# Kernel tuning notes

Measured on AMD Instinct MI355X. Metric: run time of the kernel, lower is better.

Reference implementation:

```python
import jax, jax.numpy as jnp
import numpy as np

EMB = 512
HEADS = 8
HEAD_DIM = EMB // HEADS
GN_EPS = 1e-6
THETA_SCALE = 10000.0


def _multiply_by_i(x):
    # interleave: out[..., 2i] = -x[..., 2i+1], out[..., 2i+1] = x[..., 2i]
    return jnp.stack((-x[..., 1::2], x[..., ::2]), axis=-1).reshape(x.shape)


def _theta_shift(x, sin, cos):
    return x * cos + _multiply_by_i(x) * sin


def setup_inputs() -> dict:
    key = jax.random.key(0)
    ks = jax.random.split(key, 13)
    B, N, E = 2, 2048, EMB

    def xavier(k, out_dim, in_dim):
        std = (2.0 / (out_dim + in_dim)) ** 0.5
        return std * jax.random.normal(k, (out_dim, in_dim), dtype=jnp.float32)

    return {
        "query": jax.random.normal(ks[0], (B, N, E), dtype=jnp.float32),
        "k": jax.random.normal(ks[1], (B, N, E), dtype=jnp.float32),
        "v": jax.random.normal(ks[2], (B, N, E), dtype=jnp.float32),
        "Wq": xavier(ks[3], E, E), "bq": jnp.zeros((E,), jnp.float32),
        "Wk": xavier(ks[4], E, E), "bk": jnp.zeros((E,), jnp.float32),
        "Wv": xavier(ks[5], E, E), "bv": jnp.zeros((E,), jnp.float32),
        "Wg": xavier(ks[6], E, E), "bg": jnp.zeros((E,), jnp.float32),
        "Wo": xavier(ks[7], E, E), "bo": jnp.zeros((E,), jnp.float32),
    }


def reference(query, k, v, Wq, bq, Wk, bk, Wv, bv, Wg, bg, Wo, bo):
    B, N, E = query.shape
    H, D = HEADS, E // HEADS

    def proj(x, W, b):  # torch Linear: x @ W.T + b, then split heads -> [b h n d]
        return (x @ W.T + b).reshape(B, N, H, D).transpose(0, 2, 1, 3)

    q = proj(query, Wq, bq)
    kk = proj(k, Wk, bk)
    vv = proj(v, Wv, bv)

    # rotary-style theta shift; thetas repeated pairwise [t0,t0,t1,t1,...]
    thetas = jnp.repeat(1.0 / THETA_SCALE ** jnp.linspace(0.0, 1.0, D // 2), 2)
    angles = jnp.arange(N, dtype=jnp.float32)[:, None] * thetas[None, :]  # [n d]
    sin = jnp.sin(angles)[None, None]
    cos = jnp.cos(angles)[None, None]
    q = _theta_shift(q, sin, cos)
    kk = _theta_shift(kk, sin, cos)

    # decay-masked retention (softmax-free)
    gammas = 1.0 - jnp.exp(jnp.linspace(np.log(1 / 32), np.log(1 / 512), H)).astype(jnp.float32)
    pos = jnp.arange(N)
    dist = jnp.abs(pos[:, None] - pos[None, :]).astype(jnp.float32)
    causal = pos[:, None] >= pos[None, :]
    decay_mask = jnp.where(causal[None], gammas[:, None, None] ** dist[None], 0.0)  # [h n s]

    kk = kk / (D ** 0.5)
    sim = jnp.einsum('bhnd,bhsd->bhns', q, kk) * decay_mask[None]  # [b h n n]
    ret = jnp.einsum('bhns,bhsd->bhnd', sim, vv)

    # GroupNorm(groups=H, channels=H, affine=False) over (b n) samples -> per-(b,h,n) norm over d
    mean = ret.mean(axis=-1, keepdims=True)
    var = ret.var(axis=-1, keepdims=True)
    ret = (ret - mean) / jnp.sqrt(var + GN_EPS)

    ret = ret.transpose(0, 2, 1, 3).reshape(B, N, E)
    gate = jax.nn.silu(query @ Wg.T + bg)
    out = (ret * gate) @ Wo.T + bo
    return out
```

## Files before the change

### kernel.cpp

```cpp
#include <hip/hip_runtime.h>
#include <math.h>

typedef float f32x4 __attribute__((ext_vector_type(4)));
typedef short s16x8 __attribute__((ext_vector_type(8)));
typedef short s16x4 __attribute__((ext_vector_type(4)));

__device__ __forceinline__ short f2bf(float f) {
    unsigned u = __builtin_bit_cast(unsigned, f);
    unsigned r = u + 0x7FFFu + ((u >> 16) & 1u);
    return (short)(r >> 16);
}
__device__ __forceinline__ float bf2f(short h) {
    return __builtin_bit_cast(float, ((unsigned)(unsigned short)h) << 16);
}
__device__ __forceinline__ unsigned pack2(short a, short b) {
    return (unsigned)(unsigned short)a | ((unsigned)(unsigned short)b << 16);
}

__device__ __forceinline__ void split16v(const float* __restrict__ p,
                                         short* __restrict__ h,
                                         short* __restrict__ l) {
    f32x4 a0 = *(const f32x4*)(p);
    f32x4 a1 = *(const f32x4*)(p + 4);
    f32x4 a2 = *(const f32x4*)(p + 8);
    f32x4 a3 = *(const f32x4*)(p + 12);
    #pragma unroll
    for (int i = 0; i < 4; ++i) {
        short t0;
        t0 = f2bf(a0[i]); h[i]      = t0; l[i]      = f2bf(a0[i] - bf2f(t0));
        t0 = f2bf(a1[i]); h[4 + i]  = t0; l[4 + i]  = f2bf(a1[i] - bf2f(t0));
        t0 = f2bf(a2[i]); h[8 + i]  = t0; l[8 + i]  = f2bf(a2[i] - bf2f(t0));
        t0 = f2bf(a3[i]); h[12 + i] = t0; l[12 + i] = f2bf(a3[i] - bf2f(t0));
    }
}

__device__ __forceinline__ void gload16(const void* g, void* l) {
    __builtin_amdgcn_global_load_lds(
        (const __attribute__((address_space(1))) unsigned int*)g,
        (__attribute__((address_space(3))) unsigned int*)l,
        16, 0, 0);
}

__global__ __launch_bounds__(256) void presplit_kernel(
    const float* __restrict__ W0, const float* __restrict__ W1,
    const float* __restrict__ W2, const float* __restrict__ W3,
    const float* __restrict__ W4,
    const float* __restrict__ X0, const float* __restrict__ X1,
    const float* __restrict__ X2,
    short* __restrict__ Wsp, short* __restrict__ Xsp)
{
    const int blk = blockIdx.x;
    const int t = threadIdx.x;
    short hbuf[16], lbuf[16];
    if (blk < 256) {
        const int w = blk >> 6, bi = blk & 63;
        const float* src = (w == 0) ? W0 : (w == 1) ? W1 : (w == 2) ? W2 : W3;
        const int idx = (bi * 256 + t) * 16;
        const int row = idx >> 9, k0 = idx & 511;
        const int ntile = row >> 7, r = row & 127;
        const int kstep = k0 >> 5, kk0 = k0 & 31;
        const int s = (r & 3) << 4;
        split16v(src + idx, hbuf, lbuf);
        short* hp = Wsp + (long)w * 524288 + (ntile * 16 + kstep) * 8192 + r * 32;
        short* lp = hp + 4096;
        const int oA = ((2 * kk0) ^ s) >> 1;
        const int oB = ((2 * kk0 + 16) ^ s) >> 1;
        *(s16x8*)(hp + oA) = *(s16x8*)(hbuf);
        *(s16x8*)(hp + oB) = *(s16x8*)(hbuf + 8);
        *(s16x8*)(lp + oA) = *(s16x8*)(lbuf);
        *(s16x8*)(lp + oB) = *(s16x8*)(lbuf + 8);
    } else if (blk < 320) {
        const int bi = blk - 256;
        const int idx = (bi * 256 + t) * 16;
        short* hi = Wsp + (long)4 * 524288;
        short* lo = hi + 262144;
        split16v(W4 + idx, hbuf, lbuf);
        *(s16x8*)(hi + idx)     = *(s16x8*)(hbuf);
        *(s16x8*)(hi + idx + 8) = *(s16x8*)(hbuf + 8);
        *(s16x8*)(lo + idx)     = *(s16x8*)(lbuf);
        *(s16x8*)(lo + idx + 8) = *(s16x8*)(lbuf + 8);
    } else {
        const int b2 = blk - 320;
        const int x = b2 >> 9, bi = b2 & 511;
        const float* src = (x == 0) ? X0 : (x == 1) ? X1 : X2;
        const int idx = (bi * 256 + t) * 16;
        const int row = idx >> 9, k0 = idx & 511;
        const int mtile = row >> 6, r = row & 63;
        const int kstep = k0 >> 5, kk0 = k0 & 31;
        const int s = (r & 3) << 4;
        split16v(src + idx, hbuf, lbuf);
        short* hp = Xsp + (long)x * 4194304 + (mtile * 16 + kstep) * 4096 + r * 32;
        short* lp = hp + 2048;
        const int oA = ((2 * kk0) ^ s) >> 1;
        const int oB = ((2 * kk0 + 16) ^ s) >> 1;
        *(s16x8*)(hp + oA) = *(s16x8*)(hbuf);
        *(s16x8*)(hp + oB) = *(s16x8*)(hbuf + 8);
        *(s16x8*)(lp + oA) = *(s16x8*)(lbuf);
        *(s16x8*)(lp + oB) = *(s16x8*)(lbuf + 8);
    }
}

__global__ __launch_bounds__(256, 2) void projqkvg_kernel(
    const short* __restrict__ Xsp, const short* __restrict__ Wsp,
    const float* __restrict__ bq, const float* __restrict__ bk,
    const float* __restrict__ bv, const float* __restrict__ bg,
    short* __restrict__ Qh, short* __restrict__ Ql,
    short* __restrict__ Kh, short* __restrict__ Vth,
    float* __restrict__ G)
{
    __shared__ __align__(16) short SB[36864];

    const int fid = blockIdx.x + 4 * (blockIdx.y + 64 * blockIdx.z);
    const int mtile = fid & 63;
    const int rr = fid >> 6;
    const int mode = rr & 3;
    const int ntile = rr >> 2;
    const int m0 = mtile * 64, n0 = ntile * 128;

    const int xi = (mode == 1) ? 1 : (mode == 2) ? 2 : 0;
    const float* bias = (mode == 0) ? bq : (mode == 1) ? bk
                       : (mode == 2) ? bv : bg;

    const int t = threadIdx.x, lane = t & 63, wv = t >> 6;
    const int wm = wv >> 1, wn = wv & 1;
    const int quad = lane >> 4, l15 = lane & 15;

    const short* Xblk = Xsp + (long)xi * 4194304 + (long)mtile * 16 * 4096;
    const short* Wblk = Wsp + (long)mode * 524288 + (long)ntile * 16 * 8192;

    const int c0 = wv * 6;
    const short* gs[6];
    int gstp[6];
    #pragma unroll
    for (int i = 0; i < 6; ++i) {
        const int c = c0 + i;
        const bool isx = (c < 8);
        gs[i]   = isx ? (Xblk + c * 512 + lane * 8)
                      : (Wblk + (c - 8) * 512 + lane * 8);
        gstp[i] = isx ? 4096 : 8192;
    }

    auto STAGE = [&](int stg, int ks) {
        char* dstb = (char*)SB + stg * 24576 + c0 * 1024;
        #pragma unroll
        for (int i = 0; i < 6; ++i)
            gload16(gs[i] + ks * gstp[i], dstb + i * 1024);
    };

    const int sxw = (l15 & 3) << 4;
    int aoff[2], boff[4];
    #pragma unroll
    for (int s2 = 0; s2 < 2; ++s2)
        aoff[s2] = (wm * 32 + s2 * 16 + l15) * 64 + ((quad * 16) ^ sxw);
    #pragma unroll
    for (int s2 = 0; s2 < 4; ++s2)
        boff[s2] = 8192 + (wn * 64 + s2 * 16 + l15) * 64 + ((quad * 16) ^ sxw);

    f32x4 acc[2][4];
    #pragma unroll
    for (int i = 0; i < 2; ++i)
        #pragma unroll
        for (int j = 0; j < 4; ++j)
            acc[i][j] = (f32x4){0.f, 0.f, 0.f, 0.f};

    STAGE(0, 0);
    STAGE(1, 1);
    asm volatile("s_waitcnt vmcnt(6)" ::: "memory");
    __builtin_amdgcn_s_barrier();

    int cur = 0;
    for (int ks = 0; ks < 16; ++ks) {
        if (ks < 14) {
            int fill = cur + 2; if (fill >= 3) fill -= 3;
            STAGE(fill, ks + 2);
        }
        __builtin_amdgcn_sched_barrier(0);

        const char* stg = (const char*)SB + cur * 24576;
        s16x8 ah[2], al[2], bh[4], bl[4];
        #pragma unroll
        for (int s2 = 0; s2 < 2; ++s2) {
            ah[s2] = *(const s16x8*)(stg + aoff[s2]);
            al[s2] = *(const s16x8*)(stg + 4096 + aoff[s2]);
        }
        #pragma unroll
        for (int s2 = 0; s2 < 4; ++s2) {
            bh[s2] = *(const s16x8*)(stg + boff[s2]);
            bl[s2] = *(const s16x8*)(stg + 8192 + boff[s2]);
        }
        #pragma unroll
        for (int i = 0; i < 2; ++i)
            #pragma unroll
            for (int j = 0; j < 4; ++j) {
                acc[i][j] = __builtin_amdgcn_mfma_f32_16x16x32_bf16(ah[i], bh[j], acc[i][j], 0, 0, 0);
                acc[i][j] = __builtin_amdgcn_mfma_f32_16x16x32_bf16(al[i], bh[j], acc[i][j], 0, 0, 0);
                acc[i][j] = __builtin_amdgcn_mfma_f32_16x16x32_bf16(ah[i], bl[j], acc[i][j], 0, 0, 0);
            }

        if (ks < 14)       asm volatile("s_waitcnt vmcnt(6)" ::: "memory");
        else if (ks == 14) asm volatile("s_waitcnt vmcnt(0)" ::: "memory");
        __builtin_amdgcn_sched_barrier(0);
        __builtin_amdgcn_s_barrier();

        cur += 1; if (cur >= 3) cur -= 3;
    }

    __syncthreads();

    const int bb = m0 >> 11, posb = m0 & 2047;

    if (mode == 0) {
        short* Thi = SB + wv * 2304;
        short* Tlo = Thi + 1152;
        const int hcol = (n0 >> 6) + wn;
        #pragma unroll
        for (int ms = 0; ms < 2; ++ms) {
            #pragma unroll
            for (int ns = 0; ns < 4; ++ns) {
                const int col = n0 + wn * 64 + ns * 16 + l15;
                const float bvv = bias[col];
                const int pp = (col & 63) >> 1;
                const float theta = powf(10000.0f, -(float)pp * (1.0f / 31.0f));
                #pragma unroll
                for (int r = 0; r < 4; ++r) {
                    const int m = m0 + wm * 32 + ms * 16 + quad * 4 + r;
                    const int pos = m & 2047;
                    float x = acc[ms][ns][r] + bvv;
                    float prt = __shfl_xor(x, 1);
                    float ang = (float)pos * theta;
                    float sv = sinf(ang), cv = cosf(ang);
                    float y0 = x * cv - prt * sv;
                    float y1 = prt * cv + x * sv;
                    if (!(l15 & 1)) {
                        short h0 = f2bf(y0), h1 = f2bf(y1);
                        short l0 = f2bf(y0 - bf2f(h0)), l1 = f2bf(y1 - bf2f(h1));
                        const int o = (quad * 4 + r) * 72 + ns * 16 + l15;
                        *(unsigned*)&Thi[o] = pack2(h0, h1);
                        *(unsigned*)&Tlo[o] = pack2(l0, l1);
                    }
                }
            }
            const int mrow = wm * 32 + ms * 16;
            #pragma unroll
            for (int p2 = 0; p2 < 2; ++p2) {
                const int row = p2 * 8 + (lane >> 3);
                const int ch = (lane & 7) * 8;
                s16x8 vh = *(const s16x8*)&Thi[row * 72 + ch];
                s16x8 vl = *(const s16x8*)&Tlo[row * 72 + ch];
                const long o = ((long)(bb * 8 + hcol) * 2048 + posb + mrow + row) * 64 + ch;
                *(s16x8*)(Qh + o) = vh;
                *(s16x8*)(Ql + o) = vl;
            }
        }
    } else if (mode == 1) {
        short* Thi = SB + wv * 1152;
        const int hcol = (n0 >> 6) + wn;
        #pragma unroll
        for (int ms = 0; ms < 2; ++ms) {
            #pragma unroll
            for (int ns = 0; ns < 4; ++ns) {
                const int col = n0 + wn * 64 + ns * 16 + l15;
                const float bvv = bias[col];
                const int pp = (col & 63) >> 1;
                const float theta = powf(10000.0f, -(float)pp * (1.0f / 31.0f));
                #pragma unroll
                for (int r = 0; r < 4; ++r) {
                    const int m = m0 + wm * 32 + ms * 16 + quad * 4 + r;
                    const int pos = m & 2047;
                    float x = acc[ms][ns][r] + bvv;
                    float prt = __shfl_xor(x, 1);
                    float ang = (float)pos * theta;
                    float sv = sinf(ang), cv = cosf(ang);
                    float y0 = (x * cv - prt * sv) * 0.125f;
                    float y1 = (prt * cv + x * sv) * 0.125f;
                    if (!(l15 & 1)) {
                        const int o = (quad * 4 + r) * 72 + ns * 16 + l15;
                        *(unsigned*)&Thi[o] = pack2(f2bf(y0), f2bf(y1));
                    }
                }
            }
            const int mrow = wm * 32 + ms * 16;
            #pragma unroll
            for (int p2 = 0; p2 < 2; ++p2) {
                const int row = p2 * 8 + (lane >> 3);
                const int ch = (lane & 7) * 8;
                s16x8 vh = *(const s16x8*)&Thi[row * 72 + ch];
                const long o = ((long)(bb * 8 + hcol) * 2048 + posb + mrow + row) * 64 + ch;
                *(s16x8*)(Kh + o) = vh;
            }
        }
    } else if (mode == 2) {
        short* T2 = SB;
        #pragma unroll
        for (int ns = 0; ns < 4; ++ns) {
            const int col = n0 + wn * 64 + ns * 16 + l15;
            const float bvv = bias[col];
            #pragma unroll
            for (int ms = 0; ms < 2; ++ms) {
                s16x4 pk;
                #pragma unroll
                for (int r = 0; r < 4; ++r)
                    pk[r] = f2bf(acc[ms][ns][r] + bvv);
                *(s16x4*)&T2[(wn * 64 + ns * 16 + l15) * 72
                             + wm * 32 + ms * 16 + quad * 4] = pk;
            }
        }
        __syncthreads();
        #pragma unroll
        for (int pass = 0; pass < 4; ++pass) {
            const int row = pass * 32 + (t >> 3);
            const int ch = (t & 7) * 8;
            s16x8 v = *(const s16x8*)&T2[row * 72 + ch];
            const int head = (n0 >> 6) + (row >> 6);
            const int d = row & 63;
            const long o = ((long)(bb * 8 + head) * 64 + d) * 2048 + posb + ch;
            *(s16x8*)(Vth + o) = v;
        }
    } else {
        #pragma unroll
        for (int ns = 0; ns < 4; ++ns) {
            const int col = n0 + wn * 64 + ns * 16 + l15;
            const float bvv = bias[col];
            #pragma unroll
            for (int ms = 0; ms < 2; ++ms)
                #pragma unroll
                for (int r = 0; r < 4; ++r) {
                    const int m = m0 + wm * 32 + ms * 16 + quad * 4 + r;
                    float x = acc[ms][ns][r] + bvv;
                    G[(long)m * 512 + col] = x / (1.0f + expf(-x));
                }
        }
    }
}

__global__ __launch_bounds__(256) void attn_kernel(
    const short* __restrict__ Qh_g, const short* __restrict__ Ql_g,
    const short* __restrict__ Kh_g, const short* __restrict__ Vth_g,
    const float* __restrict__ G,
    short* __restrict__ RGh)
{
    __shared__ __align__(16) short KhS[64 * 72], VhS[64 * 72];
    __shared__ __align__(16) short PhS[64 * 68];

    const int t = threadIdx.x, lane = t & 63, wv = t >> 6;
    const int quad = lane >> 4, l15 = lane & 15;
    const int bh = blockIdx.y, h = bh & 7, b = bh >> 3;
    const int qt = (bh & 1) ? blockIdx.x : (31 - blockIdx.x);
    const int n0 = qt * 64;
    const long base = (long)bh * 2048 * 64;

    float l2g;
    int stLo;
    {
        float lg0 = logf(1.0f / 32.0f), lg1 = logf(1.0f / 512.0f);
        float om = expf(lg0 + (float)h * (lg1 - lg0) * (1.0f / 7.0f));
        l2g = log2f(1.0f - om);
        int Dcut = (int)(11.5129255f / om) + 64;
        stLo = (n0 - Dcut) >> 6;
        if (stLo < 0) stLo = 0;
    }
    float gneg[16];
    #pragma unroll
    for (int i = 0; i < 16; ++i)
        gneg[i] = exp2f(-(float)((i >> 2) * 16 + (i & 3)) * l2g);

    const int srow = t >> 2;
    const int scol = (t & 3) * 16;
    const int n = n0 + wv * 16 + l15;

    s16x8 qh[2], ql[2];
    {
        const short* qp  = Qh_g + base + (long)(n0 + wv * 16 + l15) * 64 + quad * 8;
        const short* qp2 = Ql_g + base + (long)(n0 + wv * 16 + l15) * 64 + quad * 8;
        qh[0] = *(const s16x8*)qp;
        qh[1] = *(const s16x8*)(qp + 32);
        ql[0] = *(const s16x8*)qp2;
        ql[1] = *(const s16x8*)(qp2 + 32);
    }

    f32x4 racc[4];
    #pragma unroll
    for (int i = 0; i < 4; ++i) racc[i] = (f32x4){0.f, 0.f, 0.f, 0.f};

    s16x8 pk0, pk1, pv0, pv1;
    {
        const long ko = base + (long)(stLo * 64 + srow) * 64 + scol;
        pk0 = *(const s16x8*)(Kh_g + ko);
        pk1 = *(const s16x8*)(Kh_g + ko + 8);
        const long vo = base + (long)srow * 2048 + stLo * 64 + scol;
        pv0 = *(const s16x8*)(Vth_g + vo);
        pv1 = *(const s16x8*)(Vth_g + vo + 8);
    }

    for (int st = stLo; st <= qt; ++st) {
        const int s0 = st * 64;
        __syncthreads();
        *(s16x8*)&KhS[srow * 72 + scol]     = pk0;
        *(s16x8*)&KhS[srow * 72 + scol + 8] = pk1;
        *(s16x8*)&VhS[srow * 72 + scol]     = pv0;
        *(s16x8*)&VhS[srow * 72 + scol + 8] = pv1;
        __syncthreads();

        if (st < qt) {
            const long ko = base + (long)(s0 + 64 + srow) * 64 + scol;
            pk0 = *(const s16x8*)(Kh_g + ko);
            pk1 = *(const s16x8*)(Kh_g + ko + 8);
            const long vo = base + (long)srow * 2048 + s0 + 64 + scol;
            pv0 = *(const s16x8*)(Vth_g + vo);
            pv1 = *(const s16x8*)(Vth_g + vo + 8);
        }

        const float t0 = exp2f((float)(n - s0 - quad * 4) * l2g);

        #pragma unroll
        for (int sub = 0; sub < 4; ++sub) {
            const int ro = (sub * 16 + l15) * 72 + quad * 8;
            s16x8 kh0 = *(const s16x8*)&KhS[ro];
            s16x8 kh1 = *(const s16x8*)&KhS[ro + 32];
            f32x4 sacc = (f32x4){0.f, 0.f, 0.f, 0.f};
            sacc = __builtin_amdgcn_mfma_f32_16x16x32_bf16(kh0, qh[0], sacc, 0, 0, 0);
            sacc = __builtin_amdgcn_mfma_f32_16x16x32_bf16(kh1, qh[1], sacc, 0, 0, 0);
            sacc = __builtin_amdgcn_mfma_f32_16x16x32_bf16(kh0, ql[0], sacc, 0, 0, 0);
            sacc = __builtin_amdgcn_mfma_f32_16x16x32_bf16(kh1, ql[1], sacc, 0, 0, 0);

            const int sb = s0 + sub * 16 + quad * 4;
            s16x4 pkh;
            #pragma unroll
            for (int r = 0; r < 4; ++r) {
                const int s = sb + r;
                const float wgt = (n >= s) ? t0 * gneg[sub * 4 + r] : 0.0f;
                pkh[r] = f2bf(sacc[r] * wgt);
            }
            *(s16x4*)&PhS[(wv * 16 + l15) * 68 + sub * 16 + quad * 4] = pkh;
        }

        const int pro = (wv * 16 + l15) * 68 + quad * 8;
        s16x8 ph0 = *(const s16x8*)&PhS[pro];
        s16x8 ph1 = *(const s16x8*)&PhS[pro + 32];
        #pragma unroll
        for (int ds = 0; ds < 4; ++ds) {
            const int ro = (ds * 16 + l15) * 72 + quad * 8;
            s16x8 vh0 = *(const s16x8*)&VhS[ro];
            s16x8 vh1 = *(const s16x8*)&VhS[ro + 32];
            racc[ds] = __builtin_amdgcn_mfma_f32_16x16x32_bf16(ph0, vh0, racc[ds], 0, 0, 0);
            racc[ds] = __builtin_amdgcn_mfma_f32_16x16x32_bf16(ph1, vh1, racc[ds], 0, 0, 0);
        }
    }

    float mean[4], rstd[4];
    #pragma unroll
    for (int r = 0; r < 4; ++r) {
        float s = racc[0][r] + racc[1][r] + racc[2][r] + racc[3][r];
        s += __shfl_xor(s, 1); s += __shfl_xor(s, 2);
        s += __shfl_xor(s, 4); s += __shfl_xor(s, 8);
        mean[r] = s * (1.0f / 64.0f);
        float vs = 0.f;
        #pragma unroll
        for (int ds = 0; ds < 4; ++ds) {
            float d = racc[ds][r] - mean[r];
            vs += d * d;
        }
        vs += __shfl_xor(vs, 1); vs += __shfl_xor(vs, 2);
        vs += __shfl_xor(vs, 4); vs += __shfl_xor(vs, 8);
        rstd[r] = rsqrtf(vs * (1.0f / 64.0f) + 1e-6f);
    }

    __syncthreads();
    short* rgH = KhS + wv * 1152;
    #pragma unroll
    for (int ds = 0; ds < 4; ++ds) {
        #pragma unroll
        for (int r = 0; r < 4; ++r) {
            const int nn = n0 + wv * 16 + quad * 4 + r;
            const int d = ds * 16 + l15;
            const long gi = ((long)(b * 2048 + nn)) * 512 + h * 64 + d;
            float rg = (racc[ds][r] - mean[r]) * rstd[r] * G[gi];
            float prt = __shfl_xor(rg, 1);
            if (!(l15 & 1)) {
                const int o = (quad * 4 + r) * 72 + ds * 16 + l15;
                *(unsigned*)&rgH[o] = pack2(f2bf(rg), f2bf(prt));
            }
        }
    }
    #pragma unroll
    for (int p2 = 0; p2 < 2; ++p2) {
        const int row = p2 * 8 + (lane >> 3);
        const int ch = (lane & 7) * 8;
        s16x8 vh = *(const s16x8*)&rgH[row * 72 + ch];
        const int nn = n0 + wv * 16 + row;
        const long o = ((long)(b * 2048 + nn)) * 512 + h * 64 + ch;
        *(s16x8*)(RGh + o) = vh;
    }
}

__global__ __launch_bounds__(256) void projo_kernel(
    const short* __restrict__ RGh, const short* __restrict__ Woh_g,
    const float* __restrict__ bo, float* __restrict__ out)
{
    __shared__ __align__(16) char PB[23040];
    short* XhS = (short*)PB;
    short* WhS = XhS + 1280;
    short* WlS = XhS + 6400;

    const short* Wol_g = Woh_g + 262144;
    const int t = threadIdx.x, lane = t & 63, wv = t >> 6;
    const int wm = wv >> 1, wn = wv & 1;
    const int quad = lane >> 4, l15 = lane & 15;
    const int m0 = blockIdx.y * 32, n0 = blockIdx.x * 128;

    f32x4 acc[4];
    #pragma unroll
    for (int j = 0; j < 4; ++j) acc[j] = (f32x4){0.f, 0.f, 0.f, 0.f};

    const int xrow = t >> 3, xcol = (t & 7) * 4;
    const int wrow = t >> 1, wcol = (t & 1) * 16;
    const long xbase = (long)(m0 + xrow) * 512 + xcol;
    const long wbase = (long)(n0 + wrow) * 512 + wcol;

    s16x4 px;
    s16x8 pw0, pw1, pw2, pw3;
    px  = *(const s16x4*)(RGh + xbase);
    pw0 = *(const s16x8*)(Woh_g + wbase);
    pw1 = *(const s16x8*)(Woh_g + wbase + 8);
    pw2 = *(const s16x8*)(Wol_g + wbase);
    pw3 = *(const s16x8*)(Wol_g + wbase + 8);

    for (int k0 = 0; k0 < 512; k0 += 32) {
        __syncthreads();
        *(s16x4*)&XhS[xrow * 40 + xcol]     = px;
        *(s16x8*)&WhS[wrow * 40 + wcol]     = pw0;
        *(s16x8*)&WhS[wrow * 40 + wcol + 8] = pw1;
        *(s16x8*)&WlS[wrow * 40 + wcol]     = pw2;
        *(s16x8*)&WlS[wrow * 40 + wcol + 8] = pw3;
        __syncthreads();

        if (k0 + 32 < 512) {
            const long xo = xbase + k0 + 32;
            const long wo = wbase + k0 + 32;
            px  = *(const s16x4*)(RGh + xo);
            pw0 = *(const s16x8*)(Woh_g + wo);
            pw1 = *(const s16x8*)(Woh_g + wo + 8);
            pw2 = *(const s16x8*)(Wol_g + wo);
            pw3 = *(const s16x8*)(Wol_g + wo + 8);
        }

        s16x8 ah, bh[4], bl[4];
        {
            const int ro = (wm * 16 + l15) * 40 + quad * 8;
            ah = *(const s16x8*)&XhS[ro];
        }
        #pragma unroll
        for (int s = 0; s < 4; ++s) {
            const int ro = (wn * 64 + s * 16 + l15) * 40 + quad * 8;
            bh[s] = *(const s16x8*)&WhS[ro];
            bl[s] = *(const s16x8*)&WlS[ro];
        }
        #pragma unroll
        for (int j = 0; j < 4; ++j) {
            acc[j] = __builtin_amdgcn_mfma_f32_16x16x32_bf16(ah, bh[j], acc[j], 0, 0, 0);
            acc[j] = __builtin_amdgcn_mfma_f32_16x16x32_bf16(ah, bl[j], acc[j], 0, 0, 0);
        }
    }

    __syncthreads();
    float* T = (float*)PB + wv * 1152;
    #pragma unroll
    for (int ns = 0; ns < 4; ++ns) {
        const int col = n0 + wn * 64 + ns * 16 + l15;
        const float bvv = bo[col];
        #pragma unroll
        for (int r = 0; r < 4; ++r)
            T[(quad * 4 + r) * 72 + ns * 16 + l15] = acc[ns][r] + bvv;
    }
    #pragma unroll
    for (int it = 0; it < 2; ++it) {
        const int row = it * 8 + (lane >> 3);
        const int ch = (lane & 7) * 8;
        f32x4 a = *(const f32x4*)&T[row * 72 + ch];
        f32x4 c = *(const f32x4*)&T[row * 72 + ch + 4];
        const long o = (long)(m0 + wm * 16 + row) * 512 + n0 + wn * 64 + ch;
        *(f32x4*)(out + o) = a;
        *(f32x4*)(out + o + 4) = c;
    }
}

extern "C" void kernel_launch(void* const* d_in, const int* in_sizes, int n_in,
                              void* d_out, int out_size, void* d_ws, size_t ws_size,
                              hipStream_t stream) {
    const float* query = (const float*)d_in[0];
    const float* kin   = (const float*)d_in[1];
    const float* vin   = (const float*)d_in[2];
    const float* Wq = (const float*)d_in[3];
    const float* bq = (const float*)d_in[4];
    const float* Wk = (const float*)d_in[5];
    const float* bk = (const float*)d_in[6];
    const float* Wv = (const float*)d_in[7];
    const float* bv = (const float*)d_in[8];
    const float* Wg = (const float*)d_in[9];
    const float* bg = (const float*)d_in[10];
    const float* Wo = (const float*)d_in[11];
    const float* bo = (const float*)d_in[12];

    short* S = (short*)d_ws;
    const long NE = 2097152;
    short* WSp = S;
    short* Xsp = S + 2621440;
    short* Qh  = Xsp + 12582912;
    short* Ql  = Qh + NE;
    short* Kh  = Ql + NE;
    short* Vth = Kh + NE;
    float* G   = (float*)(Vth + NE);
    short* RGh = (short*)(G + NE);

    presplit_kernel<<<1856, 256, 0, stream>>>(
        Wq, Wk, Wv, Wg, Wo, query, kin, vin, WSp, Xsp);
    projqkvg_kernel<<<dim3(4, 64, 4), 256, 0, stream>>>(
        Xsp, WSp, bq, bk, bv, bg, Qh, Ql, Kh, Vth, G);
    attn_kernel<<<dim3(32, 16), 256, 0, stream>>>(
        Qh, Ql, Kh, Vth, G, RGh);
    projo_kernel<<<dim3(4, 128), 256, 0, stream>>>(
        RGh, WSp + 4 * 524288, bo, (float*)d_out);
}
```

Measured before the change: 221.0 us.

## Double projection block to 8 waves and precompute rotary sin/cos table

The QKVG projection kernel now runs 512 threads (8 waves) per block, each wave computing a 32x32 sub-tile and staging 3 instead of 6 global-to-LDS loads. MFMA sections are wrapped in s_setprio to favour matrix issue, and the per-element powf/sinf/cosf in the rotary epilogue is replaced by a lookup into a cos/sin table built by extra presplit blocks. The aim is more latency hiding and a cheaper epilogue, at the cost of an extra table read per element and a deeper per-block barrier.

```diff
diff --git a/kernel.cpp b/kernel.cpp
--- a/kernel.cpp
+++ b/kernel.cpp
@@ -47,7 +47,8 @@
     const float* __restrict__ W4,
     const float* __restrict__ X0, const float* __restrict__ X1,
     const float* __restrict__ X2,
-    short* __restrict__ Wsp, short* __restrict__ Xsp)
+    short* __restrict__ Wsp, short* __restrict__ Xsp,
+    float2* __restrict__ SC)
 {
     const int blk = blockIdx.x;
     const int t = threadIdx.x;
@@ -79,7 +80,7 @@
         *(s16x8*)(hi + idx + 8) = *(s16x8*)(hbuf + 8);
         *(s16x8*)(lo + idx)     = *(s16x8*)(lbuf);
         *(s16x8*)(lo + idx + 8) = *(s16x8*)(lbuf + 8);
-    } else {
+    } else if (blk < 1856) {
         const int b2 = blk - 320;
         const int x = b2 >> 9, bi = b2 & 511;
         const float* src = (x == 0) ? X0 : (x == 1) ? X1 : X2;
@@ -97,13 +98,20 @@
         *(s16x8*)(hp + oB) = *(s16x8*)(hbuf + 8);
         *(s16x8*)(lp + oA) = *(s16x8*)(lbuf);
         *(s16x8*)(lp + oB) = *(s16x8*)(lbuf + 8);
-    }
-}
-
-__global__ __launch_bounds__(256, 2) void projqkvg_kernel(
+    } else {
+        const int gid = (blk - 1856) * 256 + t;
+        const int pos = gid >> 5, pp = gid & 31;
+        const float theta = powf(10000.0f, -(float)pp * (1.0f / 31.0f));
+        const float ang = (float)pos * theta;
+        SC[gid] = make_float2(cosf(ang), sinf(ang));
+    }
+}
+
+__global__ __launch_bounds__(512, 4) void projqkvg_kernel(
     const short* __restrict__ Xsp, const short* __restrict__ Wsp,
     const float* __restrict__ bq, const float* __restrict__ bk,
     const float* __restrict__ bv, const float* __restrict__ bg,
+    const float2* __restrict__ SC,
     short* __restrict__ Qh, short* __restrict__ Ql,
     short* __restrict__ Kh, short* __restrict__ Vth,
     float* __restrict__ G)
@@ -122,17 +130,17 @@
                        : (mode == 2) ? bv : bg;
 
     const int t = threadIdx.x, lane = t & 63, wv = t >> 6;
-    const int wm = wv >> 1, wn = wv & 1;
+    const int wm = wv >> 2, wn = wv & 3;
     const int quad = lane >> 4, l15 = lane & 15;
 
     const short* Xblk = Xsp + (long)xi * 4194304 + (long)mtile * 16 * 4096;
     const short* Wblk = Wsp + (long)mode * 524288 + (long)ntile * 16 * 8192;
 
-    const int c0 = wv * 6;
-    const short* gs[6];
-    int gstp[6];
-    #pragma unroll
-    for (int i = 0; i < 6; ++i) {
+    const int c0 = wv * 3;
+    const short* gs[3];
+    int gstp[3];
+    #pragma unroll
+    for (int i = 0; i < 3; ++i) {
         const int c = c0 + i;
         const bool isx = (c < 8);
         gs[i]   = isx ? (Xblk + c * 512 + lane * 8)
@@ -143,29 +151,29 @@
     auto STAGE = [&](int stg, int ks) {
         char* dstb = (char*)SB + stg * 24576 + c0 * 1024;
         #pragma unroll
-        for (int i = 0; i < 6; ++i)
+        for (int i = 0; i < 3; ++i)
             gload16(gs[i] + ks * gstp[i], dstb + i * 1024);
     };
 
     const int sxw = (l15 & 3) << 4;
-    int aoff[2], boff[4];
+    int aoff[2], boff[2];
     #pragma unroll
     for (int s2 = 0; s2 < 2; ++s2)
         aoff[s2] = (wm * 32 + s2 * 16 + l15) * 64 + ((quad * 16) ^ sxw);
     #pragma unroll
-    for (int s2 = 0; s2 < 4; ++s2)
-        boff[s2] = 8192 + (wn * 64 + s2 * 16 + l15) * 64 + ((quad * 16) ^ sxw);
-
-    f32x4 acc[2][4];
+    for (int s2 = 0; s2 < 2; ++s2)
+        boff[s2] = 8192 + (wn * 32 + s2 * 16 + l15) * 64 + ((quad * 16) ^ sxw);
+
+    f32x4 acc[2][2];
     #pragma unroll
     for (int i = 0; i < 2; ++i)
         #pragma unroll
-        for (int j = 0; j < 4; ++j)
+        for (int j = 0; j < 2; ++j)
             acc[i][j] = (f32x4){0.f, 0.f, 0.f, 0.f};
 
     STAGE(0, 0);
     STAGE(1, 1);
-    asm volatile("s_waitcnt vmcnt(6)" ::: "memory");
+    asm volatile("s_waitcnt vmcnt(3)" ::: "memory");
     __builtin_amdgcn_s_barrier();
 
     int cur = 0;
@@ -177,27 +185,29 @@
         __builtin_amdgcn_sched_barrier(0);
 
         const char* stg = (const char*)SB + cur * 24576;
-        s16x8 ah[2], al[2], bh[4], bl[4];
+        s16x8 ah[2], al[2], bh[2], bl[2];
         #pragma unroll
         for (int s2 = 0; s2 < 2; ++s2) {
             ah[s2] = *(const s16x8*)(stg + aoff[s2]);
             al[s2] = *(const s16x8*)(stg + 4096 + aoff[s2]);
         }
         #pragma unroll
-        for (int s2 = 0; s2 < 4; ++s2) {
+        for (int s2 = 0; s2 < 2; ++s2) {
             bh[s2] = *(const s16x8*)(stg + boff[s2]);
             bl[s2] = *(const s16x8*)(stg + 8192 + boff[s2]);
         }
+        __builtin_amdgcn_s_setprio(1);
         #pragma unroll
         for (int i = 0; i < 2; ++i)
             #pragma unroll
-            for (int j = 0; j < 4; ++j) {
+            for (int j = 0; j < 2; ++j) {
                 acc[i][j] = __builtin_amdgcn_mfma_f32_16x16x32_bf16(ah[i], bh[j], acc[i][j], 0, 0, 0);
                 acc[i][j] = __builtin_amdgcn_mfma_f32_16x16x32_bf16(al[i], bh[j], acc[i][j], 0, 0, 0);
                 acc[i][j] = __builtin_amdgcn_mfma_f32_16x16x32_bf16(ah[i], bl[j], acc[i][j], 0, 0, 0);
             }
-
-        if (ks < 14)       asm volatile("s_waitcnt vmcnt(6)" ::: "memory");
+        __builtin_amdgcn_s_setprio(0);
+
+        if (ks < 14)       asm volatile("s_waitcnt vmcnt(3)" ::: "memory");
         else if (ks == 14) asm volatile("s_waitcnt vmcnt(0)" ::: "memory");
         __builtin_amdgcn_sched_barrier(0);
         __builtin_amdgcn_s_barrier();
@@ -210,90 +220,80 @@
     const int bb = m0 >> 11, posb = m0 & 2047;
 
     if (mode == 0) {
-        short* Thi = SB + wv * 2304;
-        short* Tlo = Thi + 1152;
-        const int hcol = (n0 >> 6) + wn;
+        short* Thi = SB + wv * 1280;
+        short* Tlo = Thi + 640;
+        const int head = (n0 >> 6) + (wn >> 1);
+        const int dbase = (wn & 1) * 32;
         #pragma unroll
         for (int ms = 0; ms < 2; ++ms) {
             #pragma unroll
-            for (int ns = 0; ns < 4; ++ns) {
-                const int col = n0 + wn * 64 + ns * 16 + l15;
+            for (int ns = 0; ns < 2; ++ns) {
+                const int col = n0 + wn * 32 + ns * 16 + l15;
                 const float bvv = bias[col];
                 const int pp = (col & 63) >> 1;
-                const float theta = powf(10000.0f, -(float)pp * (1.0f / 31.0f));
                 #pragma unroll
                 for (int r = 0; r < 4; ++r) {
                     const int m = m0 + wm * 32 + ms * 16 + quad * 4 + r;
                     const int pos = m & 2047;
                     float x = acc[ms][ns][r] + bvv;
                     float prt = __shfl_xor(x, 1);
-                    float ang = (float)pos * theta;
-                    float sv = sinf(ang), cv = cosf(ang);
-                    float y0 = x * cv - prt * sv;
-                    float y1 = prt * cv + x * sv;
+                    float2 sc = SC[pos * 32 + pp];
+                    float y0 = x * sc.x - prt * sc.y;
+                    float y1 = prt * sc.x + x * sc.y;
                     if (!(l15 & 1)) {
                         short h0 = f2bf(y0), h1 = f2bf(y1);
                         short l0 = f2bf(y0 - bf2f(h0)), l1 = f2bf(y1 - bf2f(h1));
-                        const int o = (quad * 4 + r) * 72 + ns * 16 + l15;
+                        const int o = (quad * 4 + r) * 40 + ns * 16 + l15;
                         *(unsigned*)&Thi[o] = pack2(h0, h1);
                         *(unsigned*)&Tlo[o] = pack2(l0, l1);
                     }
                 }
             }
             const int mrow = wm * 32 + ms * 16;
-            #pragma unroll
-            for (int p2 = 0; p2 < 2; ++p2) {
-                const int row = p2 * 8 + (lane >> 3);
-                const int ch = (lane & 7) * 8;
-                s16x8 vh = *(const s16x8*)&Thi[row * 72 + ch];
-                s16x8 vl = *(const s16x8*)&Tlo[row * 72 + ch];
-                const long o = ((long)(bb * 8 + hcol) * 2048 + posb + mrow + row) * 64 + ch;
-                *(s16x8*)(Qh + o) = vh;
-                *(s16x8*)(Ql + o) = vl;
-            }
+            const int row = lane >> 2, ch = (lane & 3) * 8;
+            s16x8 vh = *(const s16x8*)&Thi[row * 40 + ch];
+            s16x8 vl = *(const s16x8*)&Tlo[row * 40 + ch];
+            const long o = ((long)(bb * 8 + head) * 2048 + posb + mrow + row) * 64 + dbase + ch;
+            *(s16x8*)(Qh + o) = vh;
+            *(s16x8*)(Ql + o) = vl;
         }
     } else if (mode == 1) {
-        short* Thi = SB + wv * 1152;
-        const int hcol = (n0 >> 6) + wn;
+        short* Thi = SB + wv * 640;
+        const int head = (n0 >> 6) + (wn >> 1);
+        const int dbase = (wn & 1) * 32;
         #pragma unroll
         for (int ms = 0; ms < 2; ++ms) {
             #pragma unroll
-            for (int ns = 0; ns < 4; ++ns) {
-                const int col = n0 + wn * 64 + ns * 16 + l15;
+            for (int ns = 0; ns < 2; ++ns) {
+                const int col = n0 + wn * 32 + ns * 16 + l15;
                 const float bvv = bias[col];
                 const int pp = (col & 63) >> 1;
-                const float theta = powf(10000.0f, -(float)pp * (1.0f / 31.0f));
                 #pragma unroll
                 for (int r = 0; r < 4; ++r) {
                     const int m = m0 + wm * 32 + ms * 16 + quad * 4 + r;
                     const int pos = m & 2047;
                     float x = acc[ms][ns][r] + bvv;
                     float prt = __shfl_xor(x, 1);
-                    float ang = (float)pos * theta;
-                    float sv = sinf(ang), cv = cosf(ang);
-                    float y0 = (x * cv - prt * sv) * 0.125f;
-                    float y1 = (prt * cv + x * sv) * 0.125f;
+                    float2 sc = SC[pos * 32 + pp];
+                    float y0 = (x * sc.x - prt * sc.y) * 0.125f;
+                    float y1 = (prt * sc.x + x * sc.y) * 0.125f;
                     if (!(l15 & 1)) {
-                        const int o = (quad * 4 + r) * 72 + ns * 16 + l15;
+                        const int o = (quad * 4 + r) * 40 + ns * 16 + l15;
                         *(unsigned*)&Thi[o] = pack2(f2bf(y0), f2bf(y1));
                     }
                 }
             }
             const int mrow = wm * 32 + ms * 16;
-            #pragma unroll
-            for (int p2 = 0; p2 < 2; ++p2) {
-                const int row = p2 * 8 + (lane >> 3);
-                const int ch = (lane & 7) * 8;
-                s16x8 vh = *(const s16x8*)&Thi[row * 72 + ch];
-                const long o = ((long)(bb * 8 + hcol) * 2048 + posb + mrow + row) * 64 + ch;
-                *(s16x8*)(Kh + o) = vh;
-            }
+            const int row = lane >> 2, ch = (lane & 3) * 8;
+            s16x8 vh = *(const s16x8*)&Thi[row * 40 + ch];
+            const long o = ((long)(bb * 8 + head) * 2048 + posb + mrow + row) * 64 + dbase + ch;
+            *(s16x8*)(Kh + o) = vh;
         }
     } else if (mode == 2) {
         short* T2 = SB;
         #pragma unroll
-        for (int ns = 0; ns < 4; ++ns) {
-            const int col = n0 + wn * 64 + ns * 16 + l15;
+        for (int ns = 0; ns < 2; ++ns) {
+            const int col = n0 + wn * 32 + ns * 16 + l15;
             const float bvv = bias[col];
             #pragma unroll
             for (int ms = 0; ms < 2; ++ms) {
@@ -301,14 +301,14 @@
                 #pragma unroll
                 for (int r = 0; r < 4; ++r)
                     pk[r] = f2bf(acc[ms][ns][r] + bvv);
-                *(s16x4*)&T2[(wn * 64 + ns * 16 + l15) * 72
+                *(s16x4*)&T2[(wn * 32 + ns * 16 + l15) * 72
                              + wm * 32 + ms * 16 + quad * 4] = pk;
             }
         }
         __syncthreads();
         #pragma unroll
-        for (int pass = 0; pass < 4; ++pass) {
-            const int row = pass * 32 + (t >> 3);
+        for (int pass = 0; pass < 2; ++pass) {
+            const int row = pass * 64 + (t >> 3);
             const int ch = (t & 7) * 8;
             s16x8 v = *(const s16x8*)&T2[row * 72 + ch];
             const int head = (n0 >> 6) + (row >> 6);
@@ -318,8 +318,8 @@
         }
     } else {
         #pragma unroll
-        for (int ns = 0; ns < 4; ++ns) {
-            const int col = n0 + wn * 64 + ns * 16 + l15;
+        for (int ns = 0; ns < 2; ++ns) {
+            const int col = n0 + wn * 32 + ns * 16 + l15;
             const float bvv = bias[col];
             #pragma unroll
             for (int ms = 0; ms < 2; ++ms)
@@ -611,11 +611,12 @@
     short* Vth = Kh + NE;
     float* G   = (float*)(Vth + NE);
     short* RGh = (short*)(G + NE);
-
-    presplit_kernel<<<1856, 256, 0, stream>>>(
-        Wq, Wk, Wv, Wg, Wo, query, kin, vin, WSp, Xsp);
-    projqkvg_kernel<<<dim3(4, 64, 4), 256, 0, stream>>>(
-        Xsp, WSp, bq, bk, bv, bg, Qh, Ql, Kh, Vth, G);
+    float2* SC = (float2*)(RGh + NE);
+
+    presplit_kernel<<<2112, 256, 0, stream>>>(
+        Wq, Wk, Wv, Wg, Wo, query, kin, vin, WSp, Xsp, SC);
+    projqkvg_kernel<<<dim3(4, 64, 4), 512, 0, stream>>>(
+        Xsp, WSp, bq, bk, bv, bg, SC, Qh, Ql, Kh, Vth, G);
     attn_kernel<<<dim3(32, 16), 256, 0, stream>>>(
         Qh, Ql, Kh, Vth, G, RGh);
     projo_kernel<<<dim3(4, 128), 256, 0, stream>>>(
```

Measured after the change: 194.5 us. 12.0% less time.
